# Optimization experiments

Hardware: AMD Instinct MI355X
Metric: run time of the kernel (lower is better)

Reference implementation:

```python
import jax, jax.numpy as jnp
import numpy as np

B, L, H, N = 8, 2048, 512, 64  # batch, seq_len, d_model, SSM state size


def setup_inputs() -> dict:
    key = jax.random.key(0)
    ks = jax.random.split(key, 10)
    x = jax.random.normal(ks[0], (B, L, H), jnp.float32)
    # S4D-style parameters (diagonal SSM, S4D-Lin init)
    log_dt = jnp.log(1e-3) + jax.random.uniform(ks[1], (H,), jnp.float32) * (jnp.log(1e-1) - jnp.log(1e-3))
    A_re = -0.5 * jnp.ones((H, N), jnp.float32)
    A_im = jnp.tile(np.pi * jnp.arange(N, dtype=np.float32), (H, 1))
    C_re = jax.random.normal(ks[2], (H, N), jnp.float32) * (0.5 ** 0.5)
    C_im = jax.random.normal(ks[3], (H, N), jnp.float32) * (0.5 ** 0.5)
    D_skip = jax.random.normal(ks[4], (H,), jnp.float32)
    # S4 output linear (GLU): d_model -> 2*d_model, then gated
    W_out = jax.random.normal(ks[5], (2 * H, H), jnp.float32) / np.sqrt(H)
    b_out = jnp.zeros((2 * H,), jnp.float32)
    # LayerNorms
    g1 = jnp.ones((H,), jnp.float32); beta1 = jnp.zeros((H,), jnp.float32)
    g2 = jnp.ones((H,), jnp.float32); beta2 = jnp.zeros((H,), jnp.float32)
    # 1x1 conv FFN (kernel_size=1 => pointwise linear), d_ff = d_model
    W1 = jax.random.normal(ks[6], (H, H), jnp.float32) / np.sqrt(H)
    bc1 = jnp.zeros((H,), jnp.float32)
    W2 = jax.random.normal(ks[7], (H, H), jnp.float32) / np.sqrt(H)
    bc2 = jnp.zeros((H,), jnp.float32)
    return dict(x=x, log_dt=log_dt, A_re=A_re, A_im=A_im, C_re=C_re, C_im=C_im,
                D_skip=D_skip, W_out=W_out, b_out=b_out, g1=g1, beta1=beta1,
                g2=g2, beta2=beta2, W1=W1, bc1=bc1, W2=W2, bc2=bc2)


def _layer_norm(x, g, b):
    mu = jnp.mean(x, axis=-1, keepdims=True)
    var = jnp.mean((x - mu) ** 2, axis=-1, keepdims=True)
    return (x - mu) / jnp.sqrt(var + 1e-5) * g + b


def _s4(x, log_dt, A_re, A_im, C_re, C_im, D_skip, W_out, b_out):
    # x: (B, L, H) channels-last (transposed=False)
    Lx = x.shape[1]
    dt = jnp.exp(log_dt)                       # (H,)
    A = A_re + 1j * A_im                       # (H, N) diagonal state matrix
    dtA = A * dt[:, None]
    # ZOH discretization of C: Ct = C * (exp(dt*A) - 1) / A
    Ct = (C_re + 1j * C_im) * ((jnp.exp(dtA) - 1.0) / A)
    # Vandermonde kernel: K[h, l] = 2 Re sum_n Ct[h,n] exp(dt*A[h,n]*l)
    l = jnp.arange(Lx, dtype=jnp.float32)
    K = 2.0 * jnp.real(jnp.einsum('hn,hnl->hl', Ct, jnp.exp(dtA[:, :, None] * l)))
    # FFT long convolution (linear conv via zero-padded circular conv)
    u = jnp.swapaxes(x, 1, 2)                  # (B, H, L)
    n = 2 * Lx
    y = jnp.fft.irfft(jnp.fft.rfft(u, n) * jnp.fft.rfft(K, n)[None], n)[..., :Lx]
    y = y + D_skip[None, :, None] * u          # skip connection D*u
    y = jax.nn.gelu(y)                         # S4 default activation
    # output linear + GLU (S4 default postact)
    z = jnp.einsum('bhl,fh->bfl', y, W_out) + b_out[None, :, None]
    a, g = jnp.split(z, 2, axis=1)
    y = a * jax.nn.sigmoid(g)
    return jnp.swapaxes(y, 1, 2)               # (B, L, H)


def reference(x, log_dt, A_re, A_im, C_re, C_im, D_skip, W_out, b_out,
              g1, beta1, g2, beta2, W1, bc1, W2, bc2):
    new_x = _s4(x, log_dt, A_re, A_im, C_re, C_im, D_skip, W_out, b_out)
    x = x + new_x
    x = _layer_norm(x, g1, beta1)
    # FFN via 1x1 convs (pointwise linears); dropout is identity in eval
    y = jax.nn.relu(jnp.einsum('blh,fh->blf', x, W1) + bc1)
    y = jnp.einsum('blf,hf->blh', y, W2) + bc2
    return _layer_norm(x + y, g2, beta2)
```

## Files before the change

### kernel.cpp

```cpp
#include <hip/hip_runtime.h>
#include <cstddef>
#include <cstdint>

#define B_DIM 8
#define L_DIM 2048
#define H_DIM 512
#define N_DIM 64
#define HN (H_DIM * N_DIM)
#define BLH (B_DIM * L_DIM * H_DIM)
#define M_DIM (B_DIM * L_DIM)

typedef unsigned short u16;
typedef short bf16x8 __attribute__((ext_vector_type(8)));
typedef float floatx4 __attribute__((ext_vector_type(4)));

__device__ __forceinline__ float sigmoidf_(float v) {
    return 1.0f / (1.0f + __expf(-v));
}

__device__ __forceinline__ float gelu_tanh_(float x) {
    float x3 = x * x * x;
    float z = 0.7978845608028654f * fmaf(0.044715f, x3, x);
    float e = __expf(-2.0f * fabsf(z));
    float th = (1.0f - e) / (1.0f + e);
    th = copysignf(th, z);
    return 0.5f * x * (1.0f + th);
}

__device__ __forceinline__ u16 f2b(float f) {
    unsigned u = __float_as_uint(f);
    unsigned r = (u + 0x7fffu + ((u >> 16) & 1u)) >> 16;
    return (u16)r;
}
__device__ __forceinline__ float b2f(u16 u) {
    return __uint_as_float(((unsigned)u) << 16);
}
__device__ __forceinline__ void unpack2(unsigned u, float& a, float& b) {
    a = __uint_as_float(u << 16);
    b = __uint_as_float(u & 0xffff0000u);
}
__device__ __forceinline__ unsigned pack2(float a, float b) {
    return (unsigned)f2b(a) | ((unsigned)f2b(b) << 16);
}

__device__ __forceinline__ void csq(float& r, float& i) {
    float nr = r * r - i * i;
    i = 2.0f * r * i;
    r = nr;
}

__global__ __launch_bounds__(256) void setup_kernel(
    const float* __restrict__ x, const float* __restrict__ W_out,
    const float* __restrict__ W1, const float* __restrict__ W2,
    const float* __restrict__ log_dt, const float* __restrict__ A_re,
    const float* __restrict__ A_im, const float* __restrict__ C_re,
    const float* __restrict__ C_im, const float* __restrict__ g1,
    const float* __restrict__ beta1,
    u16* __restrict__ XT, u16* __restrict__ Wobf, u16* __restrict__ W1gbf,
    u16* __restrict__ W2bf, float* __restrict__ P, u16* __restrict__ Toep_bf,
    float* __restrict__ c1, float* __restrict__ c2)
{
    __shared__ float tile[32][33];
    __shared__ float ktab_s[4][64];
    const int bid = blockIdx.x;
    const int t   = threadIdx.x;

    if (bid < 8192) {
        int b  = bid >> 10;
        int hy = (bid >> 6) & 15;
        int lx = bid & 63;
        int l0 = lx * 32, h0 = hy * 32;
        int tx = t & 31, ty = t >> 5;
        #pragma unroll
        for (int r = 0; r < 4; ++r)
            tile[ty + r * 8][tx] = x[((size_t)b * L_DIM + l0 + ty + r * 8) * H_DIM + h0 + tx];
        __syncthreads();
        #pragma unroll
        for (int r = 0; r < 4; ++r)
            XT[(((size_t)b * H_DIM + h0 + ty + r * 8) << 11) + l0 + tx] = f2b(tile[tx][ty + r * 8]);
    } else if (bid < 9216) {
        int off = bid - 8192;
        if (off < 512) {
            int i = off * 256 + t;
            float4 v = *(const float4*)(W_out + (size_t)i * 4);
            uint2 p; p.x = pack2(v.x, v.y); p.y = pack2(v.z, v.w);
            *(uint2*)(Wobf + (size_t)i * 4) = p;
        } else if (off < 768) {
            int i = (off - 512) * 256 + t;
            float4 v = *(const float4*)(W1 + (size_t)i * 4);
            int n = (i * 4) & 511;
            float4 g = *(const float4*)(g1 + n);
            uint2 p; p.x = pack2(v.x * g.x, v.y * g.y);
            p.y = pack2(v.z * g.z, v.w * g.w);
            *(uint2*)(W1gbf + (size_t)i * 4) = p;
        } else {
            int i = (off - 768) * 256 + t;
            float4 v = *(const float4*)(W2 + (size_t)i * 4);
            uint2 p; p.x = pack2(v.x, v.y); p.y = pack2(v.z, v.w);
            *(uint2*)(W2bf + (size_t)i * 4) = p;
        }
    } else if (bid < 9344) {
        const int wv = t >> 6, lane = t & 63;
        const int i = (bid - 9216) * 256 + t;
        const int h = i >> 6;
        float dt = expf(log_dt[h]);
        float Ar = A_re[i], Ai = A_im[i];
        float ar = dt * Ar, ai = dt * Ai;
        float e = expf(ar);
        float wr = e * cosf(ai);
        float wi = e * sinf(ai);
        float em1r = wr - 1.0f, em1i = wi;
        float inv = 1.0f / fmaf(Ar, Ar, Ai * Ai);
        float qr = fmaf(em1r, Ar, em1i * Ai) * inv;
        float qi = fmaf(em1i, Ar, -(em1r * Ai)) * inv;
        float Cr = C_re[i], Ci = C_im[i];
        float c2r = 2.0f * (Cr * qr - Ci * qi);
        float c2i = 2.0f * (Cr * qi + Ci * qr);
        P[i]          = wr;
        P[HN + i]     = wi;
        P[2 * HN + i] = c2r;
        P[3 * HN + i] = c2i;

        float pr = 1.0f, pi = 0.0f;
        for (int tau = 0; tau < 64; ++tau) {
            float term = c2r * pr - c2i * pi;
            #pragma unroll
            for (int m = 32; m > 0; m >>= 1) term += __shfl_xor(term, m, 64);
            if (lane == 0) ktab_s[wv][tau] = term;
            float nr = pr * wr - pi * wi, ni = pr * wi + pi * wr;
            pr = nr; pi = ni;
        }
        __syncthreads();

        const int h0 = (bid - 9216) * 4;
        #pragma unroll
        for (int r = 0; r < 8; ++r) {
            int c = t + r * 256;
            int hh = c >> 9, rem = c & 511;
            int tt = rem >> 3, j0 = (rem & 7) * 8;
            u16 vv[8];
            #pragma unroll
            for (int jj = 0; jj < 8; ++jj) {
                int j = j0 + jj;
                vv[jj] = (j <= tt) ? f2b(ktab_s[hh][tt - j]) : (u16)0;
            }
            *(uint4*)&Toep_bf[((size_t)(h0 + hh) << 12) + (tt << 6) + j0] = *(uint4*)vv;
        }
    } else {
        int f = (bid - 9344) * 4 + (t >> 6);
        int lane = t & 63;
        int n = lane * 8;
        float4 w0 = *(const float4*)(W1 + (size_t)f * 512 + n);
        float4 w1v = *(const float4*)(W1 + (size_t)f * 512 + n + 4);
        float4 ga = *(const float4*)(g1 + n);
        float4 gb = *(const float4*)(g1 + n + 4);
        float4 b0 = *(const float4*)(beta1 + n);
        float4 b1 = *(const float4*)(beta1 + n + 4);
        float s1 = w0.x * ga.x + w0.y * ga.y + w0.z * ga.z + w0.w * ga.w
                 + w1v.x * gb.x + w1v.y * gb.y + w1v.z * gb.z + w1v.w * gb.w;
        float s2 = w0.x * b0.x + w0.y * b0.y + w0.z * b0.z + w0.w * b0.w
                 + w1v.x * b1.x + w1v.y * b1.y + w1v.z * b1.z + w1v.w * b1.w;
        #pragma unroll
        for (int m = 32; m > 0; m >>= 1) {
            s1 += __shfl_xor(s1, m, 64);
            s2 += __shfl_xor(s2, m, 64);
        }
        if (lane == 0) { c1[f] = s1; c2[f] = s2; }
    }
}

__global__ __launch_bounds__(256) void ssm_chunk_kernel(
    const u16* __restrict__ XT, const float* __restrict__ P,
    const u16* __restrict__ Toep_bf, const float* __restrict__ D_skip,
    u16* __restrict__ YT)
{
    __shared__ u16 U[128 * 72];
    __shared__ u16 S[128 * 136];
    __shared__ u16 EVT[13312];
    u16* E  = EVT;
    u16* Tp = EVT;
    u16* V  = EVT + 4608;

    const int h    = blockIdx.x;
    const int b0   = blockIdx.y * 4;
    const int t    = threadIdx.x;
    const int lane = t & 63;
    const int wv   = t >> 6;
    const int lm   = lane & 15, lq = lane >> 4;

    const int pidx = (h << 6) + lane;
    const float wr  = P[pidx],          wi  = P[HN + pidx];
    const float c2r = P[2 * HN + pidx], c2i = P[3 * HN + pidx];

    #pragma unroll
    for (int r = 0; r < 4; ++r) {
        int idx = t + r * 256;
        int row = idx >> 3, ch = idx & 7;
        const u16* gp = XT + (((size_t)(b0 + (row >> 5)) * H_DIM + h) << 11)
                           + ((row & 31) << 6) + (ch << 3);
        *(uint4*)&U[row * 72 + ch * 8] = *(const uint4*)gp;
    }

    float bwr, bwi;
    {
        float g16r = wr, g16i = wi;
        csq(g16r, g16i); csq(g16r, g16i); csq(g16r, g16i); csq(g16r, g16i);
        if (wv == 0)      { bwr = 1.0f; bwi = 0.0f; }
        else if (wv == 1) { bwr = g16r; bwi = g16i; }
        else if (wv == 2) { bwr = g16r; bwi = g16i; csq(bwr, bwi); }
        else {
            float g32r = g16r, g32i = g16i; csq(g32r, g32i);
            bwr = g32r * g16r - g32i * g16i;
            bwi = g32r * g16i + g32i * g16r;
        }
    }

    {
        float pr = bwr, pi = bwi;
        #pragma unroll
        for (int jk = 0; jk < 16; ++jk) {
            int k = (wv << 4) + jk;
            int j = 63 - k;
            E[(2 * lane) * 72 + j]     = f2b(pr);
            E[(2 * lane + 1) * 72 + j] = f2b(pi);
            float nr = pr * wr - pi * wi, ni = pr * wi + pi * wr;
            pr = nr; pi = ni;
        }
    }
    __syncthreads();

    {
        const int wm = wv >> 1, wn = wv & 1;
        floatx4 acc[4][4] = {};
        #pragma unroll
        for (int ks = 0; ks < 2; ++ks) {
            bf16x8 af[4], bfv[4];
            #pragma unroll
            for (int i = 0; i < 4; ++i)
                af[i] = *(const bf16x8*)&E[(wm * 64 + i * 16 + lm) * 72 + ks * 32 + lq * 8];
            #pragma unroll
            for (int j = 0; j < 4; ++j)
                bfv[j] = *(const bf16x8*)&U[(wn * 64 + j * 16 + lm) * 72 + ks * 32 + lq * 8];
            #pragma unroll
            for (int i = 0; i < 4; ++i) {
                #pragma unroll
                for (int j = 0; j < 4; ++j)
                    acc[i][j] = __builtin_amdgcn_mfma_f32_16x16x32_bf16(af[i], bfv[j], acc[i][j], 0, 0, 0);
            }
        }
        #pragma unroll
        for (int i = 0; i < 4; ++i) {
            #pragma unroll
            for (int j = 0; j < 4; ++j) {
                int ncol = wn * 64 + j * 16 + lm;
                int m0   = wm * 64 + i * 16 + lq * 4;
                u16 pk[4];
                #pragma unroll
                for (int r = 0; r < 4; ++r) pk[r] = f2b(acc[i][j][r]);
                *(uint2*)&S[ncol * 136 + m0] = *(uint2*)pk;
            }
        }
    }
    __syncthreads();

    {
        float pr = bwr, pi = bwi;
        {
            float nr = pr * wr - pi * wi, ni = pr * wi + pi * wr;
            pr = nr; pi = ni;
        }
        #pragma unroll
        for (int jk = 1; jk <= 16; ++jk) {
            int tr = (wv << 4) + jk - 1;
            float qr = c2r * pr - c2i * pi;
            float qi = c2r * pi + c2i * pr;
            V[tr * 136 + 2 * lane]     = f2b(qr);
            V[tr * 136 + 2 * lane + 1] = f2b(-qi);
            float nr = pr * wr - pi * wi, ni = pr * wi + pi * wr;
            pr = nr; pi = ni;
        }
        #pragma unroll
        for (int r = 0; r < 2; ++r) {
            int idx = t + r * 256;
            int row = idx >> 3, ch = idx & 7;
            *(uint4*)&Tp[row * 72 + ch * 8] =
                *(const uint4*)&Toep_bf[((size_t)h << 12) + (row << 6) + (ch << 3)];
        }
        float wTr = wr, wTi = wi;
        csq(wTr, wTi); csq(wTr, wTi); csq(wTr, wTi);
        csq(wTr, wTi); csq(wTr, wTi); csq(wTr, wTi);
        float Sr = 0.0f, Si = 0.0f;
        const int n2 = lane * 2;
        for (int c = 0; c < 32; ++c) {
            int base = (wv * 32 + c) * 136 + n2;
            unsigned lv = *(unsigned*)&S[base];
            float lr, li;
            unpack2(lv, lr, li);
            *(unsigned*)&S[base] = pack2(Sr, Si);
            float nSr = wTr * Sr - wTi * Si + lr;
            Si = wTr * Si + wTi * Sr + li;
            Sr = nSr;
        }
    }
    __syncthreads();

    {
        const float Dh = D_skip[h];
        floatx4 acc[4][2] = {};
        #pragma unroll
        for (int ks = 0; ks < 6; ++ks) {
            bf16x8 af[4], bfv[2];
            if (ks < 2) {
                #pragma unroll
                for (int i = 0; i < 4; ++i)
                    af[i] = *(const bf16x8*)&Tp[(i * 16 + lm) * 72 + ks * 32 + lq * 8];
                #pragma unroll
                for (int j = 0; j < 2; ++j)
                    bfv[j] = *(const bf16x8*)&U[(wv * 32 + j * 16 + lm) * 72 + ks * 32 + lq * 8];
            } else {
                #pragma unroll
                for (int i = 0; i < 4; ++i)
                    af[i] = *(const bf16x8*)&V[(i * 16 + lm) * 136 + (ks - 2) * 32 + lq * 8];
                #pragma unroll
                for (int j = 0; j < 2; ++j)
                    bfv[j] = *(const bf16x8*)&S[(wv * 32 + j * 16 + lm) * 136 + (ks - 2) * 32 + lq * 8];
            }
            #pragma unroll
            for (int i = 0; i < 4; ++i) {
                #pragma unroll
                for (int j = 0; j < 2; ++j)
                    acc[i][j] = __builtin_amdgcn_mfma_f32_16x16x32_bf16(af[i], bfv[j], acc[i][j], 0, 0, 0);
            }
        }
        #pragma unroll
        for (int j = 0; j < 2; ++j) {
            int ncol = wv * 32 + j * 16 + lm;
            int bloc = ncol >> 5, c = ncol & 31;
            size_t gbase = (((size_t)(b0 + bloc) * H_DIM + h) << 11) + (c << 6);
            #pragma unroll
            for (int i = 0; i < 4; ++i) {
                int t0 = i * 16 + lq * 4;
                u16 upk[4];
                *(uint2*)upk = *(const uint2*)&U[ncol * 72 + t0];
                u16 opk[4];
                #pragma unroll
                for (int r = 0; r < 4; ++r) {
                    float uvv = b2f(upk[r]);
                    float yv = gelu_tanh_(fmaf(Dh, uvv, acc[i][j][r]));
                    opk[r] = f2b(yv);
                }
                *(uint2*)&YT[gbase + t0] = *(uint2*)opk;
            }
        }
    }
}

__device__ __forceinline__ void stage_tile_512(
    const u16* __restrict__ g, u16* lds, int row0, int k0)
{
    const int t = threadIdx.x;
    const int row  = t >> 2;
    const int csrc = (t & 3) ^ ((t >> 3) & 3);
    const u16* gp = g + (size_t)(row0 + row) * 512 + k0 + csrc * 8;
    __builtin_amdgcn_global_load_lds(
        (const __attribute__((address_space(1))) unsigned int*)gp,
        (__attribute__((address_space(3))) unsigned int*)(lds + (size_t)t * 8),
        16, 0, 0);
}

__device__ __forceinline__ uint4 ldA_yt(
    const u16* __restrict__ YT, int b, int l0, int k0)
{
    const int k  = threadIdx.x >> 4;
    const int lc = threadIdx.x & 15;
    return *(const uint4*)(YT + (((size_t)(b * 512 + k0 + k)) << 11) + l0 + lc * 8);
}
__device__ __forceinline__ void dswA(u16* lds, uint4 av)
{
    const int k  = threadIdx.x >> 4;
    const int lc = threadIdx.x & 15;
    u16* p = lds + (lc * 8) * 32 + (((k >> 3) ^ (lc & 3)) << 3) + (k & 7);
    const u16* s = (const u16*)&av;
    #pragma unroll
    for (int j = 0; j < 8; ++j) p[j * 32] = s[j];
}

__global__ __launch_bounds__(512) void gemm1_glu_kernel(
    const u16* __restrict__ YT, const u16* __restrict__ Wo,
    const float* __restrict__ bo, const float* __restrict__ x,
    u16* __restrict__ out, float2* __restrict__ Pstats)
{
    __shared__ u16 As[2][128 * 32];
    __shared__ u16 Ba[2][128 * 32];
    __shared__ u16 Bg[2][128 * 32];
    __shared__ float2 red1[128][4];
    const int t    = threadIdx.x;
    const int lane = t & 63;
    const int wv   = t >> 6;
    const int wm   = wv >> 2, wn = wv & 3;
    const int lm   = lane & 15, lq = lane >> 4;
    const int sw   = (lq ^ ((lm >> 1) & 3)) * 8;
    const int m0   = blockIdx.x * 128, n0 = blockIdx.y * 128;
    const int b    = m0 >> 11;
    const int l0   = m0 & 2047;
    floatx4 accA[4][2] = {};
    floatx4 accG[4][2] = {};

    int swA[4];
    #pragma unroll
    for (int i = 0; i < 4; ++i)
        swA[i] = (lq ^ ((i * 2 + (lm >> 3)) & 3)) * 8;

    uint4 av = ldA_yt(YT, b, l0, 0);
    stage_tile_512(Wo, Ba[0], n0, 0);
    stage_tile_512(Wo, Bg[0], 512 + n0, 0);
    dswA(As[0], av);
    __syncthreads();

    int cur = 0;
    for (int k0 = 32; k0 < 512; k0 += 32) {
        const int nx = cur ^ 1;
        uint4 avn = ldA_yt(YT, b, l0, k0);
        stage_tile_512(Wo, Ba[nx], n0, k0);
        stage_tile_512(Wo, Bg[nx], 512 + n0, k0);

        bf16x8 af[4], ba[2], bg[2];
        #pragma unroll
        for (int i = 0; i < 4; ++i)
            af[i] = *(const bf16x8*)&As[cur][(wm * 64 + i * 16 + lm) * 32 + swA[i]];
        #pragma unroll
        for (int j = 0; j < 2; ++j) {
            ba[j] = *(const bf16x8*)&Ba[cur][(wn * 32 + j * 16 + lm) * 32 + sw];
            bg[j] = *(const bf16x8*)&Bg[cur][(wn * 32 + j * 16 + lm) * 32 + sw];
        }
        #pragma unroll
        for (int i = 0; i < 4; ++i) {
            #pragma unroll
            for (int j = 0; j < 2; ++j) {
                accA[i][j] = __builtin_amdgcn_mfma_f32_16x16x32_bf16(af[i], ba[j], accA[i][j], 0, 0, 0);
                accG[i][j] = __builtin_amdgcn_mfma_f32_16x16x32_bf16(af[i], bg[j], accG[i][j], 0, 0, 0);
            }
        }
        dswA(As[nx], avn);
        __syncthreads();
        cur = nx;
    }
    {
        bf16x8 af[4], ba[2], bg[2];
        #pragma unroll
        for (int i = 0; i < 4; ++i)
            af[i] = *(const bf16x8*)&As[cur][(wm * 64 + i * 16 + lm) * 32 + swA[i]];
        #pragma unroll
        for (int j = 0; j < 2; ++j) {
            ba[j] = *(const bf16x8*)&Ba[cur][(wn * 32 + j * 16 + lm) * 32 + sw];
            bg[j] = *(const bf16x8*)&Bg[cur][(wn * 32 + j * 16 + lm) * 32 + sw];
        }
        #pragma unroll
        for (int i = 0; i < 4; ++i) {
            #pragma unroll
            for (int j = 0; j < 2; ++j) {
                accA[i][j] = __builtin_amdgcn_mfma_f32_16x16x32_bf16(af[i], ba[j], accA[i][j], 0, 0, 0);
                accG[i][j] = __builtin_amdgcn_mfma_f32_16x16x32_bf16(af[i], bg[j], accG[i][j], 0, 0, 0);
            }
        }
    }

    float bav[2], bgv[2];
    #pragma unroll
    for (int j = 0; j < 2; ++j) {
        int n = n0 + wn * 32 + j * 16 + lm;
        bav[j] = bo[n]; bgv[j] = bo[512 + n];
    }
    #pragma unroll
    for (int i = 0; i < 4; ++i) {
        #pragma unroll
        for (int r = 0; r < 4; ++r) {
            int row = wm * 64 + i * 16 + lq * 4 + r;
            int m = m0 + row;
            float s = 0.0f, sq = 0.0f;
            #pragma unroll
            for (int j = 0; j < 2; ++j) {
                int n = n0 + wn * 32 + j * 16 + lm;
                float a_ = accA[i][j][r] + bav[j];
                float g_ = accG[i][j][r] + bgv[j];
                float xv = x[(size_t)m * 512 + n];
                float ov = fmaf(a_, sigmoidf_(g_), xv);
                out[(size_t)m * 512 + n] = f2b(ov);
                s += ov; sq = fmaf(ov, ov, sq);
            }
            #pragma unroll
            for (int msk = 1; msk < 16; msk <<= 1) {
                s  += __shfl_xor(s, msk, 64);
                sq += __shfl_xor(sq, msk, 64);
            }
            if (lm == 0) { float2 p; p.x = s; p.y = sq; red1[row][wn] = p; }
        }
    }
    __syncthreads();
    if (t < 128) {
        float s = 0.0f, sq = 0.0f;
        #pragma unroll
        for (int w = 0; w < 4; ++w) { float2 p = red1[t][w]; s += p.x; sq += p.y; }
        float2 o; o.x = s; o.y = sq;
        Pstats[(size_t)(m0 + t) * 4 + blockIdx.y] = o;
    }
}

__global__ __launch_bounds__(512) void gemm_relu_kernel(
    const u16* __restrict__ A, const u16* __restrict__ Bw,
    const float* __restrict__ bias, const float2* __restrict__ Pstats,
    const float* __restrict__ c1, const float* __restrict__ c2,
    u16* __restrict__ C)
{
    __shared__ u16 As[2][128 * 32];
    __shared__ u16 Bs[2][128 * 32];
    __shared__ float musig[128][2];
    const int t    = threadIdx.x;
    const int lane = t & 63;
    const int wv   = t >> 6;
    const int wm   = wv >> 2, wn = wv & 3;
    const int lm   = lane & 15, lq = lane >> 4;
    const int sw   = (lq ^ ((lm >> 1) & 3)) * 8;
    const int m0   = blockIdx.x * 128, n0 = blockIdx.y * 128;
    floatx4 acc[4][2] = {};

    if (t < 128) {
        float s = 0.0f, sq = 0.0f;
        #pragma unroll
        for (int w = 0; w < 4; ++w) {
            float2 p = Pstats[(size_t)(m0 + t) * 4 + w];
            s += p.x; sq += p.y;
        }
        float mu  = s * (1.0f / 512.0f);
        float var = sq * (1.0f / 512.0f) - mu * mu;
        musig[t][0] = mu;
        musig[t][1] = rsqrtf(var + 1e-5f);
    }
    stage_tile_512(A, As[0], m0, 0);
    stage_tile_512(Bw, Bs[0], n0, 0);
    __syncthreads();

    int cur = 0;
    for (int k0 = 32; k0 < 512; k0 += 32) {
        const int nx = cur ^ 1;
        stage_tile_512(A, As[nx], m0, k0);
        stage_tile_512(Bw, Bs[nx], n0, k0);

        bf16x8 af[4], bfr[2];
        #pragma unroll
        for (int i = 0; i < 4; ++i)
            af[i] = *(const bf16x8*)&As[cur][(wm * 64 + i * 16 + lm) * 32 + sw];
        #pragma unroll
        for (int j = 0; j < 2; ++j)
            bfr[j] = *(const bf16x8*)&Bs[cur][(wn * 32 + j * 16 + lm) * 32 + sw];
        #pragma unroll
        for (int i = 0; i < 4; ++i) {
            #pragma unroll
            for (int j = 0; j < 2; ++j)
                acc[i][j] = __builtin_amdgcn_mfma_f32_16x16x32_bf16(af[i], bfr[j], acc[i][j], 0, 0, 0);
        }
        __syncthreads();
        cur = nx;
    }
    {
        bf16x8 af[4], bfr[2];
        #pragma unroll
        for (int i = 0; i < 4; ++i)
            af[i] = *(const bf16x8*)&As[cur][(wm * 64 + i * 16 + lm) * 32 + sw];
        #pragma unroll
        for (int j = 0; j < 2; ++j)
            bfr[j] = *(const bf16x8*)&Bs[cur][(wn * 32 + j * 16 + lm) * 32 + sw];
        #pragma unroll
        for (int i = 0; i < 4; ++i) {
            #pragma unroll
            for (int j = 0; j < 2; ++j)
                acc[i][j] = __builtin_amdgcn_mfma_f32_16x16x32_bf16(af[i], bfr[j], acc[i][j], 0, 0, 0);
        }
    }
    float c1v[2], c2v[2];
    #pragma unroll
    for (int j = 0; j < 2; ++j) {
        int n = n0 + wn * 32 + j * 16 + lm;
        c1v[j] = c1[n];
        c2v[j] = c2[n] + bias[n];
    }
    #pragma unroll
    for (int i = 0; i < 4; ++i) {
        #pragma unroll
        for (int r = 0; r < 4; ++r) {
            int row = wm * 64 + i * 16 + lq * 4 + r;
            float mu = musig[row][0], rs = musig[row][1];
            float nmr = -rs * mu;
            #pragma unroll
            for (int j = 0; j < 2; ++j) {
                int n = n0 + wn * 32 + j * 16 + lm;
                float v = fmaf(rs, acc[i][j][r], fmaf(nmr, c1v[j], c2v[j]));
                C[(size_t)(m0 + row) * 512 + n] = f2b(fmaxf(v, 0.0f));
            }
        }
    }
}

__global__ __launch_bounds__(1024) void gemm2_ln_kernel(
    const u16* __restrict__ A, const u16* __restrict__ Bw,
    const float* __restrict__ bias, const u16* __restrict__ res,
    const float2* __restrict__ Pstats,
    const float* __restrict__ g1, const float* __restrict__ beta1,
    const float* __restrict__ gamma, const float* __restrict__ beta,
    float* __restrict__ out)
{
    __shared__ u16 As[2][64 * 32];
    __shared__ u16 Bs[2][512 * 32];
    __shared__ float epi[2048];
    float*  musig2 = epi;
    float2* lnred  = (float2*)epi;
    const int t    = threadIdx.x;
    const int lane = t & 63;
    const int wv   = t >> 6;
    const int lm   = lane & 15, lq = lane >> 4;
    const int sw   = (lq ^ ((lm >> 1) & 3)) * 8;
    const int m0   = blockIdx.x * 64;
    floatx4 acc[4][2] = {};

    if (t < 64) {
        float s = 0.0f, sq = 0.0f;
        #pragma unroll
        for (int w = 0; w < 4; ++w) {
            float2 p = Pstats[(size_t)(m0 + t) * 4 + w];
            s += p.x; sq += p.y;
        }
        float mu  = s * (1.0f / 512.0f);
        float var = sq * (1.0f / 512.0f) - mu * mu;
        musig2[t * 2]     = mu;
        musig2[t * 2 + 1] = rsqrtf(var + 1e-5f);
    }
    {
        #pragma unroll
        for (int r = 0; r < 2; ++r) {
            int c = t + r * 1024;
            int row = c >> 2;
            int csrc = (c & 3) ^ ((row >> 1) & 3);
            const u16* gp = Bw + (size_t)row * 512 + csrc * 8;
            __builtin_amdgcn_global_load_lds(
                (const __attribute__((address_space(1))) unsigned int*)gp,
                (__attribute__((address_space(3))) unsigned int*)(&Bs[0][0] + (size_t)c * 8),
                16, 0, 0);
        }
        if (t < 256) {
            int row = t >> 2;
            int csrc = (t & 3) ^ ((row >> 1) & 3);
            const u16* gp = A + (size_t)(m0 + row) * 512 + csrc * 8;
            __builtin_amdgcn_global_load_lds(
                (const __attribute__((address_space(1))) unsigned int*)gp,
                (__attribute__((address_space(3))) unsigned int*)(&As[0][0] + (size_t)t * 8),
                16, 0, 0);
        }
    }
    __syncthreads();

    int cur = 0;
    for (int k0 = 32; k0 < 512; k0 += 32) {
        const int nx = cur ^ 1;
        #pragma unroll
        for (int r = 0; r < 2; ++r) {
            int c = t + r * 1024;
            int row = c >> 2;
            int csrc = (c & 3) ^ ((row >> 1) & 3);
            const u16* gp = Bw + (size_t)row * 512 + k0 + csrc * 8;
            __builtin_amdgcn_global_load_lds(
                (const __attribute__((address_space(1))) unsigned int*)gp,
                (__attribute__((address_space(3))) unsigned int*)(&Bs[nx][0] + (size_t)c * 8),
                16, 0, 0);
        }
        if (t < 256) {
            int row = t >> 2;
            int csrc = (t & 3) ^ ((row >> 1) & 3);
            const u16* gp = A + (size_t)(m0 + row) * 512 + k0 + csrc * 8;
            __builtin_amdgcn_global_load_lds(
                (const __attribute__((address_space(1))) unsigned int*)gp,
                (__attribute__((address_space(3))) unsigned int*)(&As[nx][0] + (size_t)t * 8),
                16, 0, 0);
        }

        bf16x8 af[4], bfr[2];
        #pragma unroll
        for (int i = 0; i < 4; ++i)
            af[i] = *(const bf16x8*)&As[cur][(i * 16 + lm) * 32 + sw];
        #pragma unroll
        for (int j = 0; j < 2; ++j)
            bfr[j] = *(const bf16x8*)&Bs[cur][(wv * 32 + j * 16 + lm) * 32 + sw];
        #pragma unroll
        for (int i = 0; i < 4; ++i) {
            #pragma unroll
            for (int j = 0; j < 2; ++j)
                acc[i][j] = __builtin_amdgcn_mfma_f32_16x16x32_bf16(af[i], bfr[j], acc[i][j], 0, 0, 0);
        }
        __syncthreads();
        cur = nx;
    }
    {
        bf16x8 af[4], bfr[2];
        #pragma unroll
        for (int i = 0; i < 4; ++i)
            af[i] = *(const bf16x8*)&As[cur][(i * 16 + lm) * 32 + sw];
        #pragma unroll
        for (int j = 0; j < 2; ++j)
            bfr[j] = *(const bf16x8*)&Bs[cur][(wv * 32 + j * 16 + lm) * 32 + sw];
        #pragma unroll
        for (int i = 0; i < 4; ++i) {
            #pragma unroll
            for (int j = 0; j < 2; ++j)
                acc[i][j] = __builtin_amdgcn_mfma_f32_16x16x32_bf16(af[i], bfr[j], acc[i][j], 0, 0, 0);
        }
    }

    float bv[2], gv1[2], bt1[2], gv[2], btv[2];
    #pragma unroll
    for (int j = 0; j < 2; ++j) {
        int n = wv * 32 + j * 16 + lm;
        bv[j]  = bias[n];
        gv1[j] = g1[n];
        bt1[j] = beta1[n];
        gv[j]  = gamma[n];
        btv[j] = beta[n];
    }
    #pragma unroll
    for (int i = 0; i < 4; ++i) {
        #pragma unroll
        for (int r = 0; r < 4; ++r) {
            int row = i * 16 + lq * 4 + r;
            float mu1 = musig2[row * 2], rs1 = musig2[row * 2 + 1];
            int m = m0 + row;
            #pragma unroll
            for (int j = 0; j < 2; ++j) {
                int n = wv * 32 + j * 16 + lm;
                float zl = fmaf((b2f(res[(size_t)m * 512 + n]) - mu1) * rs1, gv1[j], bt1[j]);
                acc[i][j][r] += bv[j] + zl;
            }
        }
    }
    __syncthreads();

    #pragma unroll
    for (int i = 0; i < 4; ++i) {
        #pragma unroll
        for (int r = 0; r < 4; ++r) {
            float s  = acc[i][0][r] + acc[i][1][r];
            float sq = acc[i][0][r] * acc[i][0][r] + acc[i][1][r] * acc[i][1][r];
            #pragma unroll
            for (int msk = 1; msk < 16; msk <<= 1) {
                s  += __shfl_xor(s, msk, 64);
                sq += __shfl_xor(sq, msk, 64);
            }
            if (lm == 0) {
                float2 p; p.x = s; p.y = sq;
                lnred[(i * 16 + lq * 4 + r) * 16 + wv] = p;
            }
        }
    }
    __syncthreads();
    #pragma unroll
    for (int i = 0; i < 4; ++i) {
        #pragma unroll
        for (int r = 0; r < 4; ++r) {
            int row = i * 16 + lq * 4 + r;
            float s = 0.0f, sq = 0.0f;
            #pragma unroll
            for (int w = 0; w < 16; ++w) {
                float2 p = lnred[row * 16 + w];
                s += p.x; sq += p.y;
            }
            float mu  = s * (1.0f / 512.0f);
            float var = sq * (1.0f / 512.0f) - mu * mu;
            float rs  = rsqrtf(var + 1e-5f);
            #pragma unroll
            for (int j = 0; j < 2; ++j) {
                int n = wv * 32 + j * 16 + lm;
                out[(size_t)(m0 + row) * 512 + n] = fmaf((acc[i][j][r] - mu) * rs, gv[j], btv[j]);
            }
        }
    }
}

extern "C" void kernel_launch(void* const* d_in, const int* in_sizes, int n_in,
                              void* d_out, int out_size, void* d_ws, size_t ws_size,
                              hipStream_t stream)
{
    (void)in_sizes; (void)n_in; (void)out_size; (void)ws_size;
    const float* x      = (const float*)d_in[0];
    const float* log_dt = (const float*)d_in[1];
    const float* A_re   = (const float*)d_in[2];
    const float* A_im   = (const float*)d_in[3];
    const float* C_re   = (const float*)d_in[4];
    const float* C_im   = (const float*)d_in[5];
    const float* D_skip = (const float*)d_in[6];
    const float* W_out  = (const float*)d_in[7];
    const float* b_out  = (const float*)d_in[8];
    const float* g1     = (const float*)d_in[9];
    const float* beta1  = (const float*)d_in[10];
    const float* g2     = (const float*)d_in[11];
    const float* beta2  = (const float*)d_in[12];
    const float* W1     = (const float*)d_in[13];
    const float* bc1    = (const float*)d_in[14];
    const float* W2     = (const float*)d_in[15];
    const float* bc2    = (const float*)d_in[16];
    float* out = (float*)d_out;

    char*   wsb    = (char*)d_ws;
    float*  P      = (float*)wsb;
    u16*    Toep   = (u16*)(wsb + 4 * HN * 4 + 512 * 64 * 4);
    u16*    Wobf   = Toep + 512 * 4096;
    u16*    W1bf   = Wobf + 1024 * 512;
    u16*    W2bf   = W1bf + 512 * 512;
    u16*    r1     = W2bf + 512 * 512;
    u16*    r2     = r1 + BLH;
    u16*    r3     = r2 + BLH;
    float2* Pstats = (float2*)(r3 + BLH);
    float*  c1     = (float*)(Pstats + (size_t)M_DIM * 4);
    float*  c2     = c1 + 512;

    setup_kernel<<<9472, 256, 0, stream>>>(x, W_out, W1, W2, log_dt, A_re, A_im,
                                           C_re, C_im, g1, beta1,
                                           r1, Wobf, W1bf, W2bf, P, Toep, c1, c2);
    ssm_chunk_kernel<<<dim3(H_DIM, 2), 256, 0, stream>>>(r1, P, Toep, D_skip, r2);
    gemm1_glu_kernel<<<dim3(M_DIM / 128, 4), 512, 0, stream>>>(r2, Wobf, b_out, x, r3, Pstats);
    gemm_relu_kernel<<<dim3(M_DIM / 128, 4), 512, 0, stream>>>(r3, W1bf, bc1, Pstats, c1, c2, r1);
    gemm2_ln_kernel<<<M_DIM / 64, 1024, 0, stream>>>(r1, W2bf, bc2, r3, Pstats, g1, beta1, g2, beta2, out);
}
```

Before: 246.2 us.

## Split final GEMM+LayerNorm into 128x128 tiled GEMM and separate LN finish kernel

Replaces the full-row 64x512 GEMM2 block (1024 threads, whole W2 restaged per block) with 128x128 tiles that write bf16 pre-norm values and per-tile partial row statistics. A new lightweight kernel then combines the four partial stats per row and applies the second LayerNorm. The aim is to cut redundant weight traffic and improve occupancy and grid size. The cost is an extra kernel launch and a bf16 round trip of the intermediate through global memory, which also adds rounding before the final normalization.

After: 236.7 us. 1.04x faster.

```diff
diff --git a/kernel.cpp b/kernel.cpp
--- a/kernel.cpp
+++ b/kernel.cpp
@@ -601,28 +601,27 @@
     }
 }
 
-__global__ __launch_bounds__(1024) void gemm2_ln_kernel(
+__global__ __launch_bounds__(512) void gemm2_tile_kernel(
     const u16* __restrict__ A, const u16* __restrict__ Bw,
     const float* __restrict__ bias, const u16* __restrict__ res,
     const float2* __restrict__ Pstats,
     const float* __restrict__ g1, const float* __restrict__ beta1,
-    const float* __restrict__ gamma, const float* __restrict__ beta,
-    float* __restrict__ out)
-{
-    __shared__ u16 As[2][64 * 32];
-    __shared__ u16 Bs[2][512 * 32];
-    __shared__ float epi[2048];
-    float*  musig2 = epi;
-    float2* lnred  = (float2*)epi;
+    u16* __restrict__ Z, float2* __restrict__ Pstats2)
+{
+    __shared__ u16 As[2][128 * 32];
+    __shared__ u16 Bs[2][128 * 32];
+    __shared__ float musig[128][2];
+    __shared__ float2 red2[128][4];
     const int t    = threadIdx.x;
     const int lane = t & 63;
     const int wv   = t >> 6;
+    const int wm   = wv >> 2, wn = wv & 3;
     const int lm   = lane & 15, lq = lane >> 4;
     const int sw   = (lq ^ ((lm >> 1) & 3)) * 8;
-    const int m0   = blockIdx.x * 64;
+    const int m0   = blockIdx.x * 128, n0 = blockIdx.y * 128;
     floatx4 acc[4][2] = {};
 
-    if (t < 64) {
+    if (t < 128) {
         float s = 0.0f, sq = 0.0f;
         #pragma unroll
         for (int w = 0; w < 4; ++w) {
@@ -631,64 +630,26 @@
         }
         float mu  = s * (1.0f / 512.0f);
         float var = sq * (1.0f / 512.0f) - mu * mu;
-        musig2[t * 2]     = mu;
-        musig2[t * 2 + 1] = rsqrtf(var + 1e-5f);
-    }
-    {
-        #pragma unroll
-        for (int r = 0; r < 2; ++r) {
-            int c = t + r * 1024;
-            int row = c >> 2;
-            int csrc = (c & 3) ^ ((row >> 1) & 3);
-            const u16* gp = Bw + (size_t)row * 512 + csrc * 8;
-            __builtin_amdgcn_global_load_lds(
-                (const __attribute__((address_space(1))) unsigned int*)gp,
-                (__attribute__((address_space(3))) unsigned int*)(&Bs[0][0] + (size_t)c * 8),
-                16, 0, 0);
-        }
-        if (t < 256) {
-            int row = t >> 2;
-            int csrc = (t & 3) ^ ((row >> 1) & 3);
-            const u16* gp = A + (size_t)(m0 + row) * 512 + csrc * 8;
-            __builtin_amdgcn_global_load_lds(
-                (const __attribute__((address_space(1))) unsigned int*)gp,
-                (__attribute__((address_space(3))) unsigned int*)(&As[0][0] + (size_t)t * 8),
-                16, 0, 0);
-        }
-    }
+        musig[t][0] = mu;
+        musig[t][1] = rsqrtf(var + 1e-5f);
+    }
+    stage_tile_512(A, As[0], m0, 0);
+    stage_tile_512(Bw, Bs[0], n0, 0);
     __syncthreads();
 
     int cur = 0;
     for (int k0 = 32; k0 < 512; k0 += 32) {
         const int nx = cur ^ 1;
-        #pragma unroll
-        for (int r = 0; r < 2; ++r) {
-            int c = t + r * 1024;
-            int row = c >> 2;
-            int csrc = (c & 3) ^ ((row >> 1) & 3);
-            const u16* gp = Bw + (size_t)row * 512 + k0 + csrc * 8;
-            __builtin_amdgcn_global_load_lds(
-                (const __attribute__((address_space(1))) unsigned int*)gp,
-                (__attribute__((address_space(3))) unsigned int*)(&Bs[nx][0] + (size_t)c * 8),
-                16, 0, 0);
-        }
-        if (t < 256) {
-            int row = t >> 2;
-            int csrc = (t & 3) ^ ((row >> 1) & 3);
-            const u16* gp = A + (size_t)(m0 + row) * 512 + k0 + csrc * 8;
-            __builtin_amdgcn_global_load_lds(
-                (const __attribute__((address_space(1))) unsigned int*)gp,
-                (__attribute__((address_space(3))) unsigned int*)(&As[nx][0] + (size_t)t * 8),
-                16, 0, 0);
-        }
+        stage_tile_512(A, As[nx], m0, k0);
+        stage_tile_512(Bw, Bs[nx], n0, k0);
 
         bf16x8 af[4], bfr[2];
         #pragma unroll
         for (int i = 0; i < 4; ++i)
-            af[i] = *(const bf16x8*)&As[cur][(i * 16 + lm) * 32 + sw];
+            af[i] = *(const bf16x8*)&As[cur][(wm * 64 + i * 16 + lm) * 32 + sw];
         #pragma unroll
         for (int j = 0; j < 2; ++j)
-            bfr[j] = *(const bf16x8*)&Bs[cur][(wv * 32 + j * 16 + lm) * 32 + sw];
+            bfr[j] = *(const bf16x8*)&Bs[cur][(wn * 32 + j * 16 + lm) * 32 + sw];
         #pragma unroll
         for (int i = 0; i < 4; ++i) {
             #pragma unroll
@@ -702,10 +663,10 @@
         bf16x8 af[4], bfr[2];
         #pragma unroll
         for (int i = 0; i < 4; ++i)
-            af[i] = *(const bf16x8*)&As[cur][(i * 16 + lm) * 32 + sw];
+            af[i] = *(const bf16x8*)&As[cur][(wm * 64 + i * 16 + lm) * 32 + sw];
         #pragma unroll
         for (int j = 0; j < 2; ++j)
-            bfr[j] = *(const bf16x8*)&Bs[cur][(wv * 32 + j * 16 + lm) * 32 + sw];
+            bfr[j] = *(const bf16x8*)&Bs[cur][(wn * 32 + j * 16 + lm) * 32 + sw];
         #pragma unroll
         for (int i = 0; i < 4; ++i) {
             #pragma unroll
@@ -714,72 +675,81 @@
         }
     }
 
-    float bv[2], gv1[2], bt1[2], gv[2], btv[2];
+    float bv[2], gv1[2], bt1[2];
     #pragma unroll
     for (int j = 0; j < 2; ++j) {
-        int n = wv * 32 + j * 16 + lm;
+        int n = n0 + wn * 32 + j * 16 + lm;
         bv[j]  = bias[n];
         gv1[j] = g1[n];
         bt1[j] = beta1[n];
-        gv[j]  = gamma[n];
-        btv[j] = beta[n];
     }
     #pragma unroll
     for (int i = 0; i < 4; ++i) {
         #pragma unroll
         for (int r = 0; r < 4; ++r) {
-            int row = i * 16 + lq * 4 + r;
-            float mu1 = musig2[row * 2], rs1 = musig2[row * 2 + 1];
+            int row = wm * 64 + i * 16 + lq * 4 + r;
             int m = m0 + row;
+            float mu1 = musig[row][0], rs1 = musig[row][1];
+            float s = 0.0f, sq = 0.0f;
             #pragma unroll
             for (int j = 0; j < 2; ++j) {
-                int n = wv * 32 + j * 16 + lm;
+                int n = n0 + wn * 32 + j * 16 + lm;
                 float zl = fmaf((b2f(res[(size_t)m * 512 + n]) - mu1) * rs1, gv1[j], bt1[j]);
-                acc[i][j][r] += bv[j] + zl;
-            }
-        }
-    }
-    __syncthreads();
-
-    #pragma unroll
-    for (int i = 0; i < 4; ++i) {
-        #pragma unroll
-        for (int r = 0; r < 4; ++r) {
-            float s  = acc[i][0][r] + acc[i][1][r];
-            float sq = acc[i][0][r] * acc[i][0][r] + acc[i][1][r] * acc[i][1][r];
+                float v = acc[i][j][r] + bv[j] + zl;
+                Z[(size_t)m * 512 + n] = f2b(v);
+                s += v; sq = fmaf(v, v, sq);
+            }
             #pragma unroll
             for (int msk = 1; msk < 16; msk <<= 1) {
                 s  += __shfl_xor(s, msk, 64);
                 sq += __shfl_xor(sq, msk, 64);
             }
-            if (lm == 0) {
-                float2 p; p.x = s; p.y = sq;
-                lnred[(i * 16 + lq * 4 + r) * 16 + wv] = p;
-            }
+            if (lm == 0) { float2 p; p.x = s; p.y = sq; red2[row][wn] = p; }
         }
     }
     __syncthreads();
-    #pragma unroll
-    for (int i = 0; i < 4; ++i) {
-        #pragma unroll
-        for (int r = 0; r < 4; ++r) {
-            int row = i * 16 + lq * 4 + r;
-            float s = 0.0f, sq = 0.0f;
-            #pragma unroll
-            for (int w = 0; w < 16; ++w) {
-                float2 p = lnred[row * 16 + w];
-                s += p.x; sq += p.y;
-            }
-            float mu  = s * (1.0f / 512.0f);
-            float var = sq * (1.0f / 512.0f) - mu * mu;
-            float rs  = rsqrtf(var + 1e-5f);
-            #pragma unroll
-            for (int j = 0; j < 2; ++j) {
-                int n = wv * 32 + j * 16 + lm;
-                out[(size_t)(m0 + row) * 512 + n] = fmaf((acc[i][j][r] - mu) * rs, gv[j], btv[j]);
-            }
-        }
-    }
+    if (t < 128) {
+        float s = 0.0f, sq = 0.0f;
+        #pragma unroll
+        for (int w = 0; w < 4; ++w) { float2 p = red2[t][w]; s += p.x; sq += p.y; }
+        float2 o; o.x = s; o.y = sq;
+        Pstats2[(size_t)(m0 + t) * 4 + blockIdx.y] = o;
+    }
+}
+
+__global__ __launch_bounds__(256) void ln2_finish_kernel(
+    const u16* __restrict__ Z, const float2* __restrict__ Pstats2,
+    const float* __restrict__ gamma, const float* __restrict__ beta,
+    float* __restrict__ out)
+{
+    int w    = threadIdx.x >> 6;
+    int lane = threadIdx.x & 63;
+    size_t row  = (size_t)blockIdx.x * 4 + w;
+    float s = 0.0f, sq = 0.0f;
+    #pragma unroll
+    for (int w4 = 0; w4 < 4; ++w4) {
+        float2 p = Pstats2[row * 4 + w4];
+        s += p.x; sq += p.y;
+    }
+    float mu  = s * (1.0f / 512.0f);
+    float var = sq * (1.0f / 512.0f) - mu * mu;
+    float rs  = rsqrtf(var + 1e-5f);
+    size_t base = row * 512 + lane * 8;
+    uint4 raw = *(const uint4*)(Z + base);
+    float v[8];
+    unpack2(raw.x, v[0], v[1]); unpack2(raw.y, v[2], v[3]);
+    unpack2(raw.z, v[4], v[5]); unpack2(raw.w, v[6], v[7]);
+    float g[8], bt[8];
+    *(float4*)&g[0]  = *(const float4*)(gamma + lane * 8);
+    *(float4*)&g[4]  = *(const float4*)(gamma + lane * 8 + 4);
+    *(float4*)&bt[0] = *(const float4*)(beta + lane * 8);
+    *(float4*)&bt[4] = *(const float4*)(beta + lane * 8 + 4);
+    float o[8];
+    #pragma unroll
+    for (int i = 0; i < 8; ++i)
+        o[i] = fmaf((v[i] - mu) * rs, g[i], bt[i]);
+    *(float4*)(out + base)     = *(float4*)&o[0];
+    *(float4*)(out + base + 4) = *(float4*)&o[4];
 }
 
 extern "C" void kernel_launch(void* const* d_in, const int* in_sizes, int n_in,
@@ -818,6 +788,7 @@
     float2* Pstats = (float2*)(r3 + BLH);
     float*  c1     = (float*)(Pstats + (size_t)M_DIM * 4);
     float*  c2     = c1 + 512;
+    float2* Pstats2 = (float2*)(c2 + 512);
 
     setup_kernel<<<9472, 256, 0, stream>>>(x, W_out, W1, W2, log_dt, A_re, A_im,
                                            C_re, C_im, g1, beta1,
@@ -825,5 +796,6 @@
     ssm_chunk_kernel<<<dim3(H_DIM, 2), 256, 0, stream>>>(r1, P, Toep, D_skip, r2);
     gemm1_glu_kernel<<<dim3(M_DIM / 128, 4), 512, 0, stream>>>(r2, Wobf, b_out, x, r3, Pstats);
     gemm_relu_kernel<<<dim3(M_DIM / 128, 4), 512, 0, stream>>>(r3, W1bf, bc1, Pstats, c1, c2, r1);
-    gemm2_ln_kernel<<<M_DIM / 64, 1024, 0, stream>>>(r1, W2bf, bc2, r3, Pstats, g1, beta1, g2, beta2, out);
-}
+    gemm2_tile_kernel<<<dim3(M_DIM / 128, 4), 512, 0, stream>>>(r1, W2bf, bc2, r3, Pstats, g1, beta1, r2, Pstats2);
+    ln2_finish_kernel<<<M_DIM / 4, 256, 0, stream>>>(r2, Pstats2, g2, beta2, out);
+}
```
